# Optimization experiments

Measured on AMD Instinct MI355X. Metric: run time of the kernel, lower is better.

The kernel has to match this reference:

```python
import jax, jax.numpy as jnp
import numpy as np

B, T, NIN = 32, 2048, 2
H, E, M = 256, 256, 64  # hidden, embed, attention model_dim
L = 256                  # max_output_len


def setup_inputs() -> dict:
    key = jax.random.key(0)
    ks = jax.random.split(key, 20)
    s = 0.05
    sl = jnp.sort(jax.random.randint(ks[1], (B,), 1, T + 1))[::-1]
    sl = sl.at[0].set(T)  # assert: seq_lens[0] == max_seq_len
    return {
        "sequence": jax.random.normal(ks[0], (B, T, NIN), dtype=jnp.float32),
        "seq_lens": sl.astype(jnp.int32),
        "max_output_len": L,
        # encoder input projection (Linear n_in->embed)
        "Wp": jax.random.normal(ks[2], (NIN, E)) * s,
        "bp": jnp.zeros((E,), jnp.float32),
        # encoder LSTM (torch gate order i,f,g,o)
        "W_ih_e": jax.random.normal(ks[3], (4 * H, E)) * s,
        "W_hh_e": jax.random.normal(ks[4], (4 * H, H)) * s,
        "b_ih_e": jnp.zeros((4 * H,), jnp.float32),
        "b_hh_e": jnp.zeros((4 * H,), jnp.float32),
        # decoder LSTMCell (input is previous hidden, size H)
        "W_ih_d": jax.random.normal(ks[5], (4 * H, H)) * s,
        "W_hh_d": jax.random.normal(ks[6], (4 * H, H)) * s,
        "b_ih_d": jnp.zeros((4 * H,), jnp.float32),
        "b_hh_d": jnp.zeros((4 * H,), jnp.float32),
        # scaled dot attention projections (d_q->model_dim, d_k->model_dim)
        "Wq": jax.random.normal(ks[7], (H, M)) * s,
        "bq": jnp.zeros((M,), jnp.float32),
        "Wk": jax.random.normal(ks[8], (H, M)) * s,
        "bk": jnp.zeros((M,), jnp.float32),
    }


def _lstm_cell(h, c, x, W_ih, W_hh, b_ih, b_hh):
    g = x @ W_ih.T + h @ W_hh.T + b_ih + b_hh  # [B,4H]
    i, f, gg, o = jnp.split(g, 4, axis=-1)
    c = jax.nn.sigmoid(f) * c + jax.nn.sigmoid(i) * jnp.tanh(gg)
    h = jax.nn.sigmoid(o) * jnp.tanh(c)
    return h, c


def reference(sequence, seq_lens, max_output_len, Wp, bp,
              W_ih_e, W_hh_e, b_ih_e, b_hh_e,
              W_ih_d, W_hh_d, b_ih_d, b_hh_d,
              Wq, bq, Wk, bk):
    b, t, _ = sequence.shape
    emb = sequence @ Wp + bp  # [B,T,E]

    # encoder LSTM over time (packed semantics recovered below)
    def estep(carry, x_t):
        h, c = carry
        h, c = _lstm_cell(h, c, x_t, W_ih_e, W_hh_e, b_ih_e, b_hh_e)
        return (h, c), (h, c)

    h0 = jnp.zeros((b, H), sequence.dtype)
    _, (hs, cs) = jax.lax.scan(estep, (h0, h0), emb.transpose(1, 0, 2))  # [T,B,H]

    valid = jnp.arange(t)[None, :] < seq_lens[:, None]  # [B,T]
    enc = hs.transpose(1, 0, 2) * valid[..., None]  # pad_packed zeros beyond seq_len
    bidx = jnp.arange(b)
    hT = hs[seq_lens - 1, bidx]  # final hidden at each seq's last valid step
    cT = cs[seq_lens - 1, bidx]

    # decoder: precompute K projection and mask bias (constant across steps)
    kproj = enc @ Wk + bk  # [B,T,M]
    bias = jnp.where(valid, 0.0, -1e9).astype(sequence.dtype)  # [B,T]
    scale = 1.0 / jnp.sqrt(jnp.asarray(M, sequence.dtype))

    def dstep(carry, _):
        h, c = carry
        h2, c2 = _lstm_cell(h, c, h, W_ih_d, W_hh_d, b_ih_d, b_hh_d)
        q = h2 @ Wq + bq  # [B,M]
        scores = jnp.einsum('bm,btm->bt', q, kproj) * scale + bias
        probs = jax.nn.softmax(scores, axis=-1)  # [B,T]
        return (h2, c2), probs

    _, ptrs = jax.lax.scan(dstep, (hT, cT), None, length=max_output_len)  # [L,B,T]
    return ptrs.transpose(1, 0, 2)  # [B,L,T]
```

## Files before the change

kernel.cpp:

```cpp
#include <hip/hip_runtime.h>
#include <stdint.h>

#define B_ 32
#define T_ 2048
#define H_ 256
#define M_ 64
#define L_ 256
#define G4_ 1024

#define NG_ 8
#define NSL_ 16
#define EPT_ 16

#define SENT_ 0xFFFFFFFFu

__device__ __forceinline__ float sig_fast(float x){ return 1.f/(1.f+__expf(-x)); }
__device__ __forceinline__ float tanh_fast(float x){ return 2.f/(1.f+__expf(-2.f*x)) - 1.f; }
__device__ __forceinline__ float dot4(float4 a, float4 b){
  return fmaf(a.x,b.x, fmaf(a.y,b.y, fmaf(a.z,b.z, a.w*b.w)));
}

__global__ void prep_wdc(const float* __restrict__ a, const float* __restrict__ b,
                         float* __restrict__ o){
  int i = blockIdx.x*256 + threadIdx.x;
  o[i] = a[i] + b[i];
}

__global__ void prep_small(const float* __restrict__ Wp, const float* __restrict__ bp,
                           const float* __restrict__ Wihe, const float* __restrict__ bihe,
                           const float* __restrict__ bhhe, const float* __restrict__ bihd,
                           const float* __restrict__ bhhd, const float* __restrict__ Wq,
                           float* __restrict__ Wc0, float* __restrict__ Wc1,
                           float* __restrict__ bc, float* __restrict__ bdc,
                           float* __restrict__ WqT){
  int idx = blockIdx.x*256 + threadIdx.x;
  if (idx < 16384){
    int m = idx >> 8, k = idx & 255;
    WqT[m*256 + k] = Wq[k*64 + m];
  } else if (idx < 16384 + 1024){
    int j = idx - 16384;
    const float* wr = Wihe + j*256;
    float a0=0.f, a1=0.f, ab=0.f;
    for (int e=0;e<256;e++){
      float w = wr[e];
      a0 = fmaf(Wp[e],     w, a0);
      a1 = fmaf(Wp[256+e], w, a1);
      ab = fmaf(bp[e],     w, ab);
    }
    Wc0[j] = a0; Wc1[j] = a1;
    bc[j]  = ab + bihe[j] + bhhe[j];
    bdc[j] = bihd[j] + bhhd[j];
  }
}

__device__ __forceinline__ float2 poll8(const float* src){
  unsigned long long u;
  do {
    u = __hip_atomic_load((const unsigned long long*)src,
                          __ATOMIC_RELAXED, __HIP_MEMORY_SCOPE_AGENT);
  } while ((unsigned)u == SENT_ || (unsigned)(u>>32) == SENT_);
  return __builtin_bit_cast(float2, u);
}

__global__ __launch_bounds__(1024) void enc_kernel(
    const float* __restrict__ seq, const int* __restrict__ slen,
    const float* __restrict__ Whh,
    const float* __restrict__ Wc0, const float* __restrict__ Wc1,
    const float* __restrict__ bc,
    float* __restrict__ h_all, float* __restrict__ cT)
{
  const int tid = threadIdx.x;
  const int grp = blockIdx.x & 7, slice = blockIdx.x >> 3;
  const int rp = tid >> 4, kc = tid & 15;
  const int j = ((rp >> 4) << 8) + slice*EPT_ + (rp & 15);
  float4 w0 = *(const float4*)(Whh + (size_t)j*256 +   0 + kc*4);
  float4 w1 = *(const float4*)(Whh + (size_t)j*256 +  64 + kc*4);
  float4 w2 = *(const float4*)(Whh + (size_t)j*256 + 128 + kc*4);
  float4 w3 = *(const float4*)(Whh + (size_t)j*256 + 192 + kc*4);
  float c0 = Wc0[j], c1 = Wc1[j], cbv = bc[j];

  __shared__ float hbuf[4][256];
  __shared__ float sbuf[4][2];
  __shared__ float gbuf[4][64];

  const int ub = tid >> 4, ue = tid & 15;
  float creg = 0.f;
  int myb = 0, mylen = -1;
  if (tid < 64){ myb = grp + 8*ub; mylen = slen[myb]; }

  const int tb = tid >> 7, kp = tid & 127;
  const int stage_b = grp + 8*tb;

  for (int t = 0; t < T_; ++t){
    if (tid < 512){
      if (t == 0){
        *(float2*)&hbuf[tb][kp*2] = make_float2(0.f, 0.f);
      } else {
        *(float2*)&hbuf[tb][kp*2] =
            poll8(h_all + ((size_t)(t-1)*B_ + stage_b)*H_ + kp*2);
      }
      if (tid < 8) sbuf[tid>>1][tid&1] = seq[((size_t)(grp + 8*(tid>>1))*T_ + t)*2 + (tid&1)];
    }
    __syncthreads();

#pragma unroll
    for (int i = 0; i < 4; ++i){
      float4 h0 = *(const float4*)&hbuf[i][       kc*4];
      float4 h1 = *(const float4*)&hbuf[i][ 64 + kc*4];
      float4 h2 = *(const float4*)&hbuf[i][128 + kc*4];
      float4 h3 = *(const float4*)&hbuf[i][192 + kc*4];
      float a = dot4(w0,h0) + dot4(w1,h1) + dot4(w2,h2) + dot4(w3,h3);
#pragma unroll
      for (int off = 1; off < 16; off <<= 1) a += __shfl_xor(a, off);
      if (kc == 0)
        gbuf[i][rp] = fmaf(sbuf[i][0], c0, fmaf(sbuf[i][1], c1, a + cbv));
    }
    __syncthreads();

    if (tid < 64){
      float gi = gbuf[ub][      ue];
      float gf = gbuf[ub][16 + ue];
      float gg = gbuf[ub][32 + ue];
      float go = gbuf[ub][48 + ue];
      creg = sig_fast(gf)*creg + sig_fast(gi)*tanh_fast(gg);
      float h = sig_fast(go)*tanh_fast(creg);
      __hip_atomic_store(h_all + ((size_t)t*B_ + myb)*H_ + slice*EPT_ + ue, h,
                         __ATOMIC_RELAXED, __HIP_MEMORY_SCOPE_AGENT);
      if (t == mylen - 1) cT[myb*H_ + slice*EPT_ + ue] = creg;
    }
  }
}

__global__ __launch_bounds__(1024) void dec_kernel(
    const int* __restrict__ slen,
    const float* __restrict__ Wdc, const float* __restrict__ bdc,
    const float* __restrict__ h_all, const float* __restrict__ cT,
    float* __restrict__ h2_all)
{
  const int tid = threadIdx.x;
  const int grp = blockIdx.x & 7, slice = blockIdx.x >> 3;
  const int rp = tid >> 4, kc = tid & 15;
  const int j = ((rp >> 4) << 8) + slice*EPT_ + (rp & 15);
  float4 w0 = *(const float4*)(Wdc + (size_t)j*256 +   0 + kc*4);
  float4 w1 = *(const float4*)(Wdc + (size_t)j*256 +  64 + kc*4);
  float4 w2 = *(const float4*)(Wdc + (size_t)j*256 + 128 + kc*4);
  float4 w3 = *(const float4*)(Wdc + (size_t)j*256 + 192 + kc*4);
  float cbv = bdc[j];

  __shared__ float hbuf[4][256];
  __shared__ float gbuf[4][64];

  const int ub = tid >> 4, ue = tid & 15;
  float creg = 0.f; int myb = 0;
  if (tid < 64){ myb = grp + 8*ub; creg = cT[myb*H_ + slice*EPT_ + ue]; }

  const int tb = tid >> 7, kp = tid & 127;
  const int stage_b = grp + 8*tb;
  int stage_len = 1;
  if (tid < 512) stage_len = slen[stage_b];

  for (int s = 0; s < L_; ++s){
    if (tid < 512){
      if (s == 0){
        *(float2*)&hbuf[tb][kp*2] =
            *(const float2*)(h_all + ((size_t)(stage_len-1)*B_ + stage_b)*H_ + kp*2);
      } else {
        *(float2*)&hbuf[tb][kp*2] =
            poll8(h2_all + ((size_t)(s-1)*B_ + stage_b)*H_ + kp*2);
      }
    }
    __syncthreads();

#pragma unroll
    for (int i = 0; i < 4; ++i){
      float4 h0 = *(const float4*)&hbuf[i][       kc*4];
      float4 h1 = *(const float4*)&hbuf[i][ 64 + kc*4];
      float4 h2 = *(const float4*)&hbuf[i][128 + kc*4];
      float4 h3 = *(const float4*)&hbuf[i][192 + kc*4];
      float a = dot4(w0,h0) + dot4(w1,h1) + dot4(w2,h2) + dot4(w3,h3);
#pragma unroll
      for (int off = 1; off < 16; off <<= 1) a += __shfl_xor(a, off);
      if (kc == 0) gbuf[i][rp] = a + cbv;
    }
    __syncthreads();

    if (tid < 64){
      float gi = gbuf[ub][      ue];
      float gf = gbuf[ub][16 + ue];
      float gg = gbuf[ub][32 + ue];
      float go = gbuf[ub][48 + ue];
      creg = sig_fast(gf)*creg + sig_fast(gi)*tanh_fast(gg);
      float h = sig_fast(go)*tanh_fast(creg);
      __hip_atomic_store(h2_all + ((size_t)s*B_ + myb)*H_ + slice*EPT_ + ue, h,
                         __ATOMIC_RELAXED, __HIP_MEMORY_SCOPE_AGENT);
    }
  }
}

__global__ __launch_bounds__(256) void kproj_kernel(
    const float* __restrict__ h_all, const int* __restrict__ slen,
    const float* __restrict__ Wk, const float* __restrict__ bk,
    float* __restrict__ kp)
{
  __shared__ float wk[256*64];
  const int tid = threadIdx.x;
  const int b = blockIdx.x >> 4, tc = blockIdx.x & 15;
  const int t0 = tc*128;
#pragma unroll
  for (int i=0;i<16;i++){
    int idx = tid + i*256;
    *(float4*)(&wk[idx*4]) = *(const float4*)(Wk + idx*4);
  }
  __syncthreads();
  const int tp = tid>>2, mc = (tid&3)*16;
  const int ta = t0 + tp*2, tb = ta+1;
  const int len = slen[b];
  const bool va = ta < len, vb = tb < len;
  const float* ha = h_all + ((size_t)ta*B_ + b)*H_;
  const float* hb = h_all + ((size_t)tb*B_ + b)*H_;
  float4 A[4], Bv[4];
#pragma unroll
  for (int u=0;u<4;u++){ A[u].x=A[u].y=A[u].z=A[u].w=0.f; Bv[u]=A[u]; }

  for (int k4=0;k4<64;k4++){
    float xa[4], xb[4];
    if (va){ float4 v = *(const float4*)(ha + k4*4); xa[0]=v.x; xa[1]=v.y; xa[2]=v.z; xa[3]=v.w; }
    else   { xa[0]=xa[1]=xa[2]=xa[3]=0.f; }
    if (vb){ float4 v = *(const float4*)(hb + k4*4); xb[0]=v.x; xb[1]=v.y; xb[2]=v.z; xb[3]=v.w; }
    else   { xb[0]=xb[1]=xb[2]=xb[3]=0.f; }
#pragma unroll
    for (int jj=0;jj<4;jj++){
      const float* wr = &wk[(k4*4+jj)*64 + mc];
#pragma unroll
      for (int u=0;u<4;u++){
        float4 wv = *(const float4*)(wr + u*4);
        A[u].x  = fmaf(xa[jj],wv.x,A[u].x);  A[u].y  = fmaf(xa[jj],wv.y,A[u].y);
        A[u].z  = fmaf(xa[jj],wv.z,A[u].z);  A[u].w  = fmaf(xa[jj],wv.w,A[u].w);
        Bv[u].x = fmaf(xb[jj],wv.x,Bv[u].x); Bv[u].y = fmaf(xb[jj],wv.y,Bv[u].y);
        Bv[u].z = fmaf(xb[jj],wv.z,Bv[u].z); Bv[u].w = fmaf(xb[jj],wv.w,Bv[u].w);
      }
    }
  }
#pragma unroll
  for (int u=0;u<4;u++){
    float4 bkv = *(const float4*)(bk + mc + u*4);
    float4 ra, rb;
    ra.x = va ? A[u].x+bkv.x : bkv.x;  ra.y = va ? A[u].y+bkv.y : bkv.y;
    ra.z = va ? A[u].z+bkv.z : bkv.z;  ra.w = va ? A[u].w+bkv.w : bkv.w;
    rb.x = vb ? Bv[u].x+bkv.x : bkv.x; rb.y = vb ? Bv[u].y+bkv.y : bkv.y;
    rb.z = vb ? Bv[u].z+bkv.z : bkv.z; rb.w = vb ? Bv[u].w+bkv.w : bkv.w;
    *(float4*)(kp + ((size_t)b*T_+ta)*M_ + mc + u*4) = ra;
    *(float4*)(kp + ((size_t)b*T_+tb)*M_ + mc + u*4) = rb;
  }
}

__global__ __launch_bounds__(256) void attn_kernel(
    const float* __restrict__ h2_all, const float* __restrict__ kp,
    const float* __restrict__ WqT, const float* __restrict__ bq,
    const int* __restrict__ slen, float* __restrict__ out)
{
  const int tid = threadIdx.x;
  const int b = blockIdx.x >> 5, scg = blockIdx.x & 31;
  const int s0 = scg*8;
  __shared__ float qL[8][64];
  __shared__ float red[8][4];
  const int wid = tid>>6, lane = tid&63;

  {
    const int jj = tid>>5, mh = tid&31;
    const float* hr = h2_all + ((size_t)(s0+jj)*B_ + b)*H_;
    const float* wa = WqT + (size_t)mh*256;
    const float* wb = WqT + (size_t)(mh+32)*256;
    float a0=0.f, a1=0.f;
    for (int k4=0;k4<64;k4++){
      float4 h4 = *(const float4*)(hr + k4*4);
      float4 v0 = *(const float4*)(wa + k4*4);
      float4 v1 = *(const float4*)(wb + k4*4);
      a0 += dot4(h4,v0);
      a1 += dot4(h4,v1);
    }
    qL[jj][mh]    = a0 + bq[mh];
    qL[jj][mh+32] = a1 + bq[mh+32];
  }
  __syncthreads();

  const int len = slen[b];
  float sc_[8][8];
#pragma unroll
  for (int ti=0; ti<8; ti++){
    const int t = ti*256 + tid;
    const float* kr = kp + ((size_t)b*T_ + t)*M_;
    float tmp[8];
#pragma unroll
    for (int jj=0;jj<8;jj++) tmp[jj]=0.f;
#pragma unroll
    for (int u4=0; u4<4; u4++){
      float4 k0 = *(const float4*)(kr + u4*16);
      float4 k1 = *(const float4*)(kr + u4*16 + 4);
      float4 k2 = *(const float4*)(kr + u4*16 + 8);
      float4 k3 = *(const float4*)(kr + u4*16 + 12);
#pragma unroll
      for (int jj=0;jj<8;jj++){
        const float4* q4 = (const float4*)&qL[jj][u4*16];
        tmp[jj] += dot4(k0,q4[0]) + dot4(k1,q4[1]) + dot4(k2,q4[2]) + dot4(k3,q4[3]);
      }
    }
    float bias = (t<len) ? 0.f : -1e9f;
#pragma unroll
    for (int jj=0;jj<8;jj++) sc_[ti][jj] = fmaf(tmp[jj], 0.125f, bias);
  }

  float mx[8];
#pragma unroll
  for (int jj=0;jj<8;jj++){
    float m = sc_[0][jj];
#pragma unroll
    for (int ti=1;ti<8;ti++) m = fmaxf(m, sc_[ti][jj]);
#pragma unroll
    for (int off=1; off<64; off<<=1) m = fmaxf(m, __shfl_xor(m, off));
    if (lane==0) red[jj][wid] = m;
  }
  __syncthreads();
#pragma unroll
  for (int jj=0;jj<8;jj++)
    mx[jj] = fmaxf(fmaxf(red[jj][0],red[jj][1]), fmaxf(red[jj][2],red[jj][3]));
  __syncthreads();
#pragma unroll
  for (int jj=0;jj<8;jj++){
    float s = 0.f;
#pragma unroll
    for (int ti=0;ti<8;ti++){
      float e = __expf(sc_[ti][jj] - mx[jj]);
      sc_[ti][jj] = e;
      s += e;
    }
#pragma unroll
    for (int off=1; off<64; off<<=1) s += __shfl_xor(s, off);
    if (lane==0) red[jj][wid] = s;
  }
  __syncthreads();
#pragma unroll
  for (int jj=0;jj<8;jj++){
    float r = 1.f/(red[jj][0]+red[jj][1]+red[jj][2]+red[jj][3]);
    float* o = out + ((size_t)b*L_ + s0 + jj)*T_;
#pragma unroll
    for (int ti=0;ti<8;ti++) o[ti*256 + tid] = sc_[ti][jj]*r;
  }
}

extern "C" void kernel_launch(void* const* d_in, const int* in_sizes, int n_in,
                              void* d_out, int out_size, void* d_ws, size_t ws_size,
                              hipStream_t stream) {
  (void)in_sizes; (void)n_in; (void)out_size;
  const float* seq  = (const float*)d_in[0];
  const int*   slen = (const int*)  d_in[1];
  const float* Wp   = (const float*)d_in[3];
  const float* bp   = (const float*)d_in[4];
  const float* Wihe = (const float*)d_in[5];
  const float* Whhe = (const float*)d_in[6];
  const float* bihe = (const float*)d_in[7];
  const float* bhhe = (const float*)d_in[8];
  const float* Wihd = (const float*)d_in[9];
  const float* Whhd = (const float*)d_in[10];
  const float* bihd = (const float*)d_in[11];
  const float* bhhd = (const float*)d_in[12];
  const float* Wq   = (const float*)d_in[13];
  const float* bq   = (const float*)d_in[14];
  const float* Wk   = (const float*)d_in[15];
  const float* bk   = (const float*)d_in[16];
  float* out = (float*)d_out;

  char* p = (char*)d_ws;
  auto take = [&](size_t bytes)->char* {
    char* r = p; p += (bytes + 255) & ~(size_t)255; return r;
  };
  float* h2_all = (float*)take((size_t)L_*B_*H_*4);
  float* kproj  = (float*)take((size_t)B_*T_*M_*4);
  float* cT     = (float*)take((size_t)B_*H_*4);
  float* W_dc   = (float*)take((size_t)G4_*H_*4);
  float* Wc0    = (float*)take(G4_*4);
  float* Wc1    = (float*)take(G4_*4);
  float* bc     = (float*)take(G4_*4);
  float* b_dc   = (float*)take(G4_*4);
  float* WqT    = (float*)take((size_t)M_*H_*4);

  size_t used = (size_t)(p - (char*)d_ws);
  float* h_all;
  if (ws_size >= used + (size_t)T_*B_*H_*4) {
    h_all = (float*)take((size_t)T_*B_*H_*4);
  } else {
    h_all = out;
  }

  hipMemsetAsync(h_all,  0xFF, (size_t)T_*B_*H_*4, stream);
  hipMemsetAsync(h2_all, 0xFF, (size_t)L_*B_*H_*4, stream);

  prep_wdc  <<<G4_*H_/256, 256, 0, stream>>>(Wihd, Whhd, W_dc);
  prep_small<<<68, 256, 0, stream>>>(Wp, bp, Wihe, bihe, bhhe, bihd, bhhd, Wq,
                                     Wc0, Wc1, bc, b_dc, WqT);
  enc_kernel<<<NG_*NSL_, 1024, 0, stream>>>(seq, slen, Whhe, Wc0, Wc1, bc,
                                            h_all, cT);
  kproj_kernel<<<B_*16, 256, 0, stream>>>(h_all, slen, Wk, bk, kproj);
  dec_kernel<<<NG_*NSL_, 1024, 0, stream>>>(slen, W_dc, b_dc, h_all, cT, h2_all);
  attn_kernel<<<B_*32, 256, 0, stream>>>(h2_all, kproj, WqT, bq, slen, out);
}
```

Baseline: 7.475 ms.

## Replace sentinel polling on full history with step-tagged ring buffers

The encoder and decoder recurrences previously polled the full h_all/h2_all histories for a 0xFF sentinel, which required memsetting about 72 MB before each run. Each step's hidden state is now also published into a small per-group ring of 64-bit words tagging the value with its step index, and readers spin on that tag. Results are still written to h_all/h2_all with plain stores for the downstream kernels. This removes the large memsets and keeps the polled data in a small, L2-resident region, at the cost of 1024 threads polling 8-byte words each step instead of 512 threads.

```diff
diff --git a/kernel.cpp b/kernel.cpp
--- a/kernel.cpp
+++ b/kernel.cpp
@@ -11,8 +11,7 @@
 #define NG_ 8
 #define NSL_ 16
 #define EPT_ 16
-
-#define SENT_ 0xFFFFFFFFu
+#define RING_ 8
 
 __device__ __forceinline__ float sig_fast(float x){ return 1.f/(1.f+__expf(-x)); }
 __device__ __forceinline__ float tanh_fast(float x){ return 2.f/(1.f+__expf(-2.f*x)) - 1.f; }
@@ -53,21 +52,13 @@
   }
 }
 
-__device__ __forceinline__ float2 poll8(const float* src){
-  unsigned long long u;
-  do {
-    u = __hip_atomic_load((const unsigned long long*)src,
-                          __ATOMIC_RELAXED, __HIP_MEMORY_SCOPE_AGENT);
-  } while ((unsigned)u == SENT_ || (unsigned)(u>>32) == SENT_);
-  return __builtin_bit_cast(float2, u);
-}
-
 __global__ __launch_bounds__(1024) void enc_kernel(
     const float* __restrict__ seq, const int* __restrict__ slen,
     const float* __restrict__ Whh,
     const float* __restrict__ Wc0, const float* __restrict__ Wc1,
     const float* __restrict__ bc,
-    float* __restrict__ h_all, float* __restrict__ cT)
+    float* __restrict__ h_all, float* __restrict__ cT,
+    unsigned long long* __restrict__ ring)
 {
   const int tid = threadIdx.x;
   const int grp = blockIdx.x & 7, slice = blockIdx.x >> 3;
@@ -88,19 +79,20 @@
   int myb = 0, mylen = -1;
   if (tid < 64){ myb = grp + 8*ub; mylen = slen[myb]; }
 
-  const int tb = tid >> 7, kp = tid & 127;
-  const int stage_b = grp + 8*tb;
+  const int ib = tid >> 8, ik = tid & 255;
+  unsigned long long* ringg = ring + (size_t)grp * (RING_*1024);
 
   for (int t = 0; t < T_; ++t){
-    if (tid < 512){
-      if (t == 0){
-        *(float2*)&hbuf[tb][kp*2] = make_float2(0.f, 0.f);
-      } else {
-        *(float2*)&hbuf[tb][kp*2] =
-            poll8(h_all + ((size_t)(t-1)*B_ + stage_b)*H_ + kp*2);
-      }
-      if (tid < 8) sbuf[tid>>1][tid&1] = seq[((size_t)(grp + 8*(tid>>1))*T_ + t)*2 + (tid&1)];
-    }
+    if (t == 0){
+      hbuf[ib][ik] = 0.f;
+    } else {
+      const unsigned long long* pp = ringg + (size_t)((t-1) & (RING_-1))*1024 + tid;
+      unsigned long long v;
+      do { v = __hip_atomic_load(pp, __ATOMIC_RELAXED, __HIP_MEMORY_SCOPE_AGENT); }
+      while ((unsigned)(v >> 32) != (unsigned)t);
+      hbuf[ib][ik] = __uint_as_float((unsigned)v);
+    }
+    if (tid < 8) sbuf[tid>>1][tid&1] = seq[((size_t)(grp + 8*(tid>>1))*T_ + t)*2 + (tid&1)];
     __syncthreads();
 
 #pragma unroll
@@ -124,8 +116,11 @@
       float go = gbuf[ub][48 + ue];
       creg = sig_fast(gf)*creg + sig_fast(gi)*tanh_fast(gg);
       float h = sig_fast(go)*tanh_fast(creg);
-      __hip_atomic_store(h_all + ((size_t)t*B_ + myb)*H_ + slice*EPT_ + ue, h,
-                         __ATOMIC_RELAXED, __HIP_MEMORY_SCOPE_AGENT);
+      unsigned long long pk = ((unsigned long long)(unsigned)(t+1) << 32)
+                            | (unsigned long long)__float_as_uint(h);
+      __hip_atomic_store(ringg + (size_t)(t & (RING_-1))*1024 + ub*256 + slice*EPT_ + ue,
+                         pk, __ATOMIC_RELAXED, __HIP_MEMORY_SCOPE_AGENT);
+      h_all[((size_t)t*B_ + myb)*H_ + slice*EPT_ + ue] = h;
       if (t == mylen - 1) cT[myb*H_ + slice*EPT_ + ue] = creg;
     }
   }
@@ -135,7 +130,7 @@
     const int* __restrict__ slen,
     const float* __restrict__ Wdc, const float* __restrict__ bdc,
     const float* __restrict__ h_all, const float* __restrict__ cT,
-    float* __restrict__ h2_all)
+    float* __restrict__ h2_all, unsigned long long* __restrict__ ring)
 {
   const int tid = threadIdx.x;
   const int grp = blockIdx.x & 7, slice = blockIdx.x >> 3;
@@ -154,20 +149,20 @@
   float creg = 0.f; int myb = 0;
   if (tid < 64){ myb = grp + 8*ub; creg = cT[myb*H_ + slice*EPT_ + ue]; }
 
-  const int tb = tid >> 7, kp = tid & 127;
-  const int stage_b = grp + 8*tb;
-  int stage_len = 1;
-  if (tid < 512) stage_len = slen[stage_b];
+  const int ib = tid >> 8, ik = tid & 255;
+  const int stage_b = grp + 8*ib;
+  const int stage_len = slen[stage_b];
+  unsigned long long* ringg = ring + (size_t)grp * (RING_*1024);
 
   for (int s = 0; s < L_; ++s){
-    if (tid < 512){
-      if (s == 0){
-        *(float2*)&hbuf[tb][kp*2] =
-            *(const float2*)(h_all + ((size_t)(stage_len-1)*B_ + stage_b)*H_ + kp*2);
-      } else {
-        *(float2*)&hbuf[tb][kp*2] =
-            poll8(h2_all + ((size_t)(s-1)*B_ + stage_b)*H_ + kp*2);
-      }
+    if (s == 0){
+      hbuf[ib][ik] = h_all[((size_t)(stage_len-1)*B_ + stage_b)*H_ + ik];
+    } else {
+      const unsigned long long* pp = ringg + (size_t)((s-1) & (RING_-1))*1024 + tid;
+      unsigned long long v;
+      do { v = __hip_atomic_load(pp, __ATOMIC_RELAXED, __HIP_MEMORY_SCOPE_AGENT); }
+      while ((unsigned)(v >> 32) != (unsigned)s);
+      hbuf[ib][ik] = __uint_as_float((unsigned)v);
     }
     __syncthreads();
 
@@ -191,8 +186,11 @@
       float go = gbuf[ub][48 + ue];
       creg = sig_fast(gf)*creg + sig_fast(gi)*tanh_fast(gg);
       float h = sig_fast(go)*tanh_fast(creg);
-      __hip_atomic_store(h2_all + ((size_t)s*B_ + myb)*H_ + slice*EPT_ + ue, h,
-                         __ATOMIC_RELAXED, __HIP_MEMORY_SCOPE_AGENT);
+      unsigned long long pk = ((unsigned long long)(unsigned)(s+1) << 32)
+                            | (unsigned long long)__float_as_uint(h);
+      __hip_atomic_store(ringg + (size_t)(s & (RING_-1))*1024 + ub*256 + slice*EPT_ + ue,
+                         pk, __ATOMIC_RELAXED, __HIP_MEMORY_SCOPE_AGENT);
+      h2_all[((size_t)s*B_ + myb)*H_ + slice*EPT_ + ue] = h;
     }
   }
 }
@@ -383,6 +381,8 @@
   float* bc     = (float*)take(G4_*4);
   float* b_dc   = (float*)take(G4_*4);
   float* WqT    = (float*)take((size_t)M_*H_*4);
+  unsigned long long* ring_e = (unsigned long long*)take((size_t)NG_*RING_*1024*8);
+  unsigned long long* ring_d = (unsigned long long*)take((size_t)NG_*RING_*1024*8);
 
   size_t used = (size_t)(p - (char*)d_ws);
   float* h_all;
@@ -392,15 +392,16 @@
     h_all = out;
   }
 
-  hipMemsetAsync(h_all,  0xFF, (size_t)T_*B_*H_*4, stream);
-  hipMemsetAsync(h2_all, 0xFF, (size_t)L_*B_*H_*4, stream);
+  hipMemsetAsync(ring_e, 0, (size_t)NG_*RING_*1024*8, stream);
+  hipMemsetAsync(ring_d, 0, (size_t)NG_*RING_*1024*8, stream);
 
   prep_wdc  <<<G4_*H_/256, 256, 0, stream>>>(Wihd, Whhd, W_dc);
   prep_small<<<68, 256, 0, stream>>>(Wp, bp, Wihe, bihe, bhhe, bihd, bhhd, Wq,
                                      Wc0, Wc1, bc, b_dc, WqT);
   enc_kernel<<<NG_*NSL_, 1024, 0, stream>>>(seq, slen, Whhe, Wc0, Wc1, bc,
-                                            h_all, cT);
+                                            h_all, cT, ring_e);
   kproj_kernel<<<B_*16, 256, 0, stream>>>(h_all, slen, Wk, bk, kproj);
-  dec_kernel<<<NG_*NSL_, 1024, 0, stream>>>(slen, W_dc, b_dc, h_all, cT, h2_all);
+  dec_kernel<<<NG_*NSL_, 1024, 0, stream>>>(slen, W_dc, b_dc, h_all, cT,
+                                            h2_all, ring_d);
   attn_kernel<<<B_*32, 256, 0, stream>>>(h2_all, kproj, WqT, bq, slen, out);
 }
```

New measurement: 6.799 ms. -9.0%, faster.

## Replace sentinel polling with flag-based ring buffer exchange in recurrent LSTM kernels

Applied to the files above, without the earlier changes.

The encoder and decoder recurrences stop spinning on sentinel values in the full hidden-state history. Each block now publishes its hidden slice into a small ring buffer in global memory and raises a per-producer flag with release semantics. Consumers wait on the flags with acquire, then do one relaxed read per element, and the block's own slice is taken from shared memory. This removes the large sentinel memsets and the per-element spin loads, but adds extra barriers per step and relies on flag-ordering correctness across the ring.

```diff
diff --git a/kernel.cpp b/kernel.cpp
--- a/kernel.cpp
+++ b/kernel.cpp
@@ -11,8 +11,7 @@
 #define NG_ 8
 #define NSL_ 16
 #define EPT_ 16
-
-#define SENT_ 0xFFFFFFFFu
+#define RING_ 8
 
 __device__ __forceinline__ float sig_fast(float x){ return 1.f/(1.f+__expf(-x)); }
 __device__ __forceinline__ float tanh_fast(float x){ return 2.f/(1.f+__expf(-2.f*x)) - 1.f; }
@@ -53,21 +52,13 @@
   }
 }
 
-__device__ __forceinline__ float2 poll8(const float* src){
-  unsigned long long u;
-  do {
-    u = __hip_atomic_load((const unsigned long long*)src,
-                          __ATOMIC_RELAXED, __HIP_MEMORY_SCOPE_AGENT);
-  } while ((unsigned)u == SENT_ || (unsigned)(u>>32) == SENT_);
-  return __builtin_bit_cast(float2, u);
-}
-
 __global__ __launch_bounds__(1024) void enc_kernel(
     const float* __restrict__ seq, const int* __restrict__ slen,
     const float* __restrict__ Whh,
     const float* __restrict__ Wc0, const float* __restrict__ Wc1,
     const float* __restrict__ bc,
-    float* __restrict__ h_all, float* __restrict__ cT)
+    float* __restrict__ h_all, float* __restrict__ cT,
+    unsigned long long* __restrict__ rde, int* __restrict__ flge)
 {
   const int tid = threadIdx.x;
   const int grp = blockIdx.x & 7, slice = blockIdx.x >> 3;
@@ -82,6 +73,7 @@
   __shared__ float hbuf[4][256];
   __shared__ float sbuf[4][2];
   __shared__ float gbuf[4][64];
+  __shared__ float xbuf[4][16];
 
   const int ub = tid >> 4, ue = tid & 15;
   float creg = 0.f;
@@ -89,45 +81,80 @@
   if (tid < 64){ myb = grp + 8*ub; mylen = slen[myb]; }
 
   const int tb = tid >> 7, kp = tid & 127;
-  const int stage_b = grp + 8*tb;
-
-  for (int t = 0; t < T_; ++t){
-    if (tid < 512){
-      if (t == 0){
-        *(float2*)&hbuf[tb][kp*2] = make_float2(0.f, 0.f);
-      } else {
-        *(float2*)&hbuf[tb][kp*2] =
-            poll8(h_all + ((size_t)(t-1)*B_ + stage_b)*H_ + kp*2);
-      }
-      if (tid < 8) sbuf[tid>>1][tid&1] = seq[((size_t)(grp + 8*(tid>>1))*T_ + t)*2 + (tid&1)];
-    }
-    __syncthreads();
-
-#pragma unroll
-    for (int i = 0; i < 4; ++i){
-      float4 h0 = *(const float4*)&hbuf[i][       kc*4];
-      float4 h1 = *(const float4*)&hbuf[i][ 64 + kc*4];
-      float4 h2 = *(const float4*)&hbuf[i][128 + kc*4];
-      float4 h3 = *(const float4*)&hbuf[i][192 + kc*4];
-      float a = dot4(w0,h0) + dot4(w1,h1) + dot4(w2,h2) + dot4(w3,h3);
-#pragma unroll
-      for (int off = 1; off < 16; off <<= 1) a += __shfl_xor(a, off);
-      if (kc == 0)
-        gbuf[i][rp] = fmaf(sbuf[i][0], c0, fmaf(sbuf[i][1], c1, a + cbv));
-    }
-    __syncthreads();
-
-    if (tid < 64){
+  const int ps = (tid - 64) >> 2, pb = (tid - 64) & 3;
+
+  for (int i = 0; i < T_; ++i){
+    const int slot = (i - 1) & (RING_ - 1);
+    if (i > 0 && tid < 64){
       float gi = gbuf[ub][      ue];
       float gf = gbuf[ub][16 + ue];
       float gg = gbuf[ub][32 + ue];
       float go = gbuf[ub][48 + ue];
       creg = sig_fast(gf)*creg + sig_fast(gi)*tanh_fast(gg);
       float h = sig_fast(go)*tanh_fast(creg);
-      __hip_atomic_store(h_all + ((size_t)t*B_ + myb)*H_ + slice*EPT_ + ue, h,
-                         __ATOMIC_RELAXED, __HIP_MEMORY_SCOPE_AGENT);
-      if (t == mylen - 1) cT[myb*H_ + slice*EPT_ + ue] = creg;
-    }
+      xbuf[ub][ue] = h;
+      hbuf[ub][slice*EPT_ + ue] = h;
+      h_all[((size_t)(i-1)*B_ + myb)*H_ + slice*EPT_ + ue] = h;
+      if (i == mylen) cT[myb*H_ + slice*EPT_ + ue] = creg;
+    }
+    __syncthreads();
+
+    if (i > 0 && tid < 4){
+      unsigned long long* dst = rde + (((size_t)slot*NG_ + grp)*4 + tid)*128 + slice*8;
+      const unsigned long long* xs = (const unsigned long long*)xbuf[tid];
+#pragma unroll
+      for (int k = 0; k < 8; ++k)
+        __hip_atomic_store(dst + k, xs[k], __ATOMIC_RELAXED, __HIP_MEMORY_SCOPE_AGENT);
+      int* fp = flge + ((((size_t)slot*NG_ + grp)*NSL_ + slice)*4 + tid)*16;
+      __hip_atomic_store(fp, i, __ATOMIC_RELEASE, __HIP_MEMORY_SCOPE_AGENT);
+    }
+    if (i > 0 && tid >= 64 && tid < 128 && ps != slice){
+      const int* fp = flge + ((((size_t)slot*NG_ + grp)*NSL_ + ps)*4 + pb)*16;
+      while (__hip_atomic_load(fp, __ATOMIC_RELAXED, __HIP_MEMORY_SCOPE_AGENT) != i) {}
+      __builtin_amdgcn_fence(__ATOMIC_ACQUIRE, "agent");
+    }
+    if (tid >= 128 && tid < 136){
+      int b4 = (tid - 128) >> 1, ix = (tid - 128) & 1;
+      sbuf[b4][ix] = seq[((size_t)(grp + 8*b4)*T_ + i)*2 + ix];
+    }
+    __syncthreads();
+
+    if (tid < 512){
+      if (i == 0){
+        *(float2*)&hbuf[tb][kp*2] = make_float2(0.f, 0.f);
+      } else if ((kp >> 3) != slice){
+        unsigned long long v = __hip_atomic_load(
+            rde + (((size_t)slot*NG_ + grp)*4 + tb)*128 + kp,
+            __ATOMIC_RELAXED, __HIP_MEMORY_SCOPE_AGENT);
+        *(float2*)&hbuf[tb][kp*2] = __builtin_bit_cast(float2, v);
+      }
+    }
+    __syncthreads();
+
+#pragma unroll
+    for (int b4 = 0; b4 < 4; ++b4){
+      float4 h0 = *(const float4*)&hbuf[b4][       kc*4];
+      float4 h1 = *(const float4*)&hbuf[b4][ 64 + kc*4];
+      float4 h2 = *(const float4*)&hbuf[b4][128 + kc*4];
+      float4 h3 = *(const float4*)&hbuf[b4][192 + kc*4];
+      float a = dot4(w0,h0) + dot4(w1,h1) + dot4(w2,h2) + dot4(w3,h3);
+#pragma unroll
+      for (int off = 1; off < 16; off <<= 1) a += __shfl_xor(a, off);
+      if (kc == 0)
+        gbuf[b4][rp] = fmaf(sbuf[b4][0], c0, fmaf(sbuf[b4][1], c1, a + cbv));
+    }
+    __syncthreads();
+  }
+
+  if (tid < 64){
+    float gi = gbuf[ub][      ue];
+    float gf = gbuf[ub][16 + ue];
+    float gg = gbuf[ub][32 + ue];
+    float go = gbuf[ub][48 + ue];
+    creg = sig_fast(gf)*creg + sig_fast(gi)*tanh_fast(gg);
+    float h = sig_fast(go)*tanh_fast(creg);
+    h_all[((size_t)(T_-1)*B_ + myb)*H_ + slice*EPT_ + ue] = h;
+    if (mylen == T_) cT[myb*H_ + slice*EPT_ + ue] = creg;
   }
 }
 
@@ -135,7 +162,8 @@
     const int* __restrict__ slen,
     const float* __restrict__ Wdc, const float* __restrict__ bdc,
     const float* __restrict__ h_all, const float* __restrict__ cT,
-    float* __restrict__ h2_all)
+    float* __restrict__ h2_all,
+    unsigned long long* __restrict__ rdd, int* __restrict__ flgd)
 {
   const int tid = threadIdx.x;
   const int grp = blockIdx.x & 7, slice = blockIdx.x >> 3;
@@ -149,6 +177,7 @@
 
   __shared__ float hbuf[4][256];
   __shared__ float gbuf[4][64];
+  __shared__ float xbuf[4][16];
 
   const int ub = tid >> 4, ue = tid & 15;
   float creg = 0.f; int myb = 0;
@@ -158,42 +187,74 @@
   const int stage_b = grp + 8*tb;
   int stage_len = 1;
   if (tid < 512) stage_len = slen[stage_b];
-
-  for (int s = 0; s < L_; ++s){
-    if (tid < 512){
-      if (s == 0){
-        *(float2*)&hbuf[tb][kp*2] =
-            *(const float2*)(h_all + ((size_t)(stage_len-1)*B_ + stage_b)*H_ + kp*2);
-      } else {
-        *(float2*)&hbuf[tb][kp*2] =
-            poll8(h2_all + ((size_t)(s-1)*B_ + stage_b)*H_ + kp*2);
-      }
-    }
-    __syncthreads();
-
-#pragma unroll
-    for (int i = 0; i < 4; ++i){
-      float4 h0 = *(const float4*)&hbuf[i][       kc*4];
-      float4 h1 = *(const float4*)&hbuf[i][ 64 + kc*4];
-      float4 h2 = *(const float4*)&hbuf[i][128 + kc*4];
-      float4 h3 = *(const float4*)&hbuf[i][192 + kc*4];
-      float a = dot4(w0,h0) + dot4(w1,h1) + dot4(w2,h2) + dot4(w3,h3);
-#pragma unroll
-      for (int off = 1; off < 16; off <<= 1) a += __shfl_xor(a, off);
-      if (kc == 0) gbuf[i][rp] = a + cbv;
-    }
-    __syncthreads();
-
-    if (tid < 64){
+  const int ps = (tid - 64) >> 2, pb = (tid - 64) & 3;
+
+  for (int i = 0; i < L_; ++i){
+    const int slot = (i - 1) & (RING_ - 1);
+    if (i > 0 && tid < 64){
       float gi = gbuf[ub][      ue];
       float gf = gbuf[ub][16 + ue];
       float gg = gbuf[ub][32 + ue];
       float go = gbuf[ub][48 + ue];
       creg = sig_fast(gf)*creg + sig_fast(gi)*tanh_fast(gg);
       float h = sig_fast(go)*tanh_fast(creg);
-      __hip_atomic_store(h2_all + ((size_t)s*B_ + myb)*H_ + slice*EPT_ + ue, h,
-                         __ATOMIC_RELAXED, __HIP_MEMORY_SCOPE_AGENT);
-    }
+      xbuf[ub][ue] = h;
+      hbuf[ub][slice*EPT_ + ue] = h;
+      h2_all[((size_t)(i-1)*B_ + myb)*H_ + slice*EPT_ + ue] = h;
+    }
+    __syncthreads();
+
+    if (i > 0 && tid < 4){
+      unsigned long long* dst = rdd + (((size_t)slot*NG_ + grp)*4 + tid)*128 + slice*8;
+      const unsigned long long* xs = (const unsigned long long*)xbuf[tid];
+#pragma unroll
+      for (int k = 0; k < 8; ++k)
+        __hip_atomic_store(dst + k, xs[k], __ATOMIC_RELAXED, __HIP_MEMORY_SCOPE_AGENT);
+      int* fp = flgd + ((((size_t)slot*NG_ + grp)*NSL_ + slice)*4 + tid)*16;
+      __hip_atomic_store(fp, i, __ATOMIC_RELEASE, __HIP_MEMORY_SCOPE_AGENT);
+    }
+    if (i > 0 && tid >= 64 && tid < 128 && ps != slice){
+      const int* fp = flgd + ((((size_t)slot*NG_ + grp)*NSL_ + ps)*4 + pb)*16;
+      while (__hip_atomic_load(fp, __ATOMIC_RELAXED, __HIP_MEMORY_SCOPE_AGENT) != i) {}
+      __builtin_amdgcn_fence(__ATOMIC_ACQUIRE, "agent");
+    }
+    __syncthreads();
+
+    if (tid < 512){
+      if (i == 0){
+        *(float2*)&hbuf[tb][kp*2] =
+            *(const float2*)(h_all + ((size_t)(stage_len-1)*B_ + stage_b)*H_ + kp*2);
+      } else if ((kp >> 3) != slice){
+        unsigned long long v = __hip_atomic_load(
+            rdd + (((size_t)slot*NG_ + grp)*4 + tb)*128 + kp,
+            __ATOMIC_RELAXED, __HIP_MEMORY_SCOPE_AGENT);
+        *(float2*)&hbuf[tb][kp*2] = __builtin_bit_cast(float2, v);
+      }
+    }
+    __syncthreads();
+
+#pragma unroll
+    for (int b4 = 0; b4 < 4; ++b4){
+      float4 h0 = *(const float4*)&hbuf[b4][       kc*4];
+      float4 h1 = *(const float4*)&hbuf[b4][ 64 + kc*4];
+      float4 h2 = *(const float4*)&hbuf[b4][128 + kc*4];
+      float4 h3 = *(const float4*)&hbuf[b4][192 + kc*4];
+      float a = dot4(w0,h0) + dot4(w1,h1) + dot4(w2,h2) + dot4(w3,h3);
+#pragma unroll
+      for (int off = 1; off < 16; off <<= 1) a += __shfl_xor(a, off);
+      if (kc == 0) gbuf[b4][rp] = a + cbv;
+    }
+    __syncthreads();
+  }
+
+  if (tid < 64){
+    float gi = gbuf[ub][      ue];
+    float gf = gbuf[ub][16 + ue];
+    float gg = gbuf[ub][32 + ue];
+    float go = gbuf[ub][48 + ue];
+    creg = sig_fast(gf)*creg + sig_fast(gi)*tanh_fast(gg);
+    float h = sig_fast(go)*tanh_fast(creg);
+    h2_all[((size_t)(L_-1)*B_ + myb)*H_ + slice*EPT_ + ue] = h;
   }
 }
 
@@ -383,6 +444,10 @@
   float* bc     = (float*)take(G4_*4);
   float* b_dc   = (float*)take(G4_*4);
   float* WqT    = (float*)take((size_t)M_*H_*4);
+  unsigned long long* rde = (unsigned long long*)take((size_t)RING_*NG_*4*128*8);
+  unsigned long long* rdd = (unsigned long long*)take((size_t)RING_*NG_*4*128*8);
+  int* flge = (int*)take((size_t)RING_*NG_*NSL_*4*16*4);
+  int* flgd = (int*)take((size_t)RING_*NG_*NSL_*4*16*4);
 
   size_t used = (size_t)(p - (char*)d_ws);
   float* h_all;
@@ -392,15 +457,16 @@
     h_all = out;
   }
 
-  hipMemsetAsync(h_all,  0xFF, (size_t)T_*B_*H_*4, stream);
-  hipMemsetAsync(h2_all, 0xFF, (size_t)L_*B_*H_*4, stream);
+  hipMemsetAsync(flge, 0, (size_t)RING_*NG_*NSL_*4*16*4, stream);
+  hipMemsetAsync(flgd, 0, (size_t)RING_*NG_*NSL_*4*16*4, stream);
 
   prep_wdc  <<<G4_*H_/256, 256, 0, stream>>>(Wihd, Whhd, W_dc);
   prep_small<<<68, 256, 0, stream>>>(Wp, bp, Wihe, bihe, bhhe, bihd, bhhd, Wq,
                                      Wc0, Wc1, bc, b_dc, WqT);
   enc_kernel<<<NG_*NSL_, 1024, 0, stream>>>(seq, slen, Whhe, Wc0, Wc1, bc,
-                                            h_all, cT);
+                                            h_all, cT, rde, flge);
   kproj_kernel<<<B_*16, 256, 0, stream>>>(h_all, slen, Wk, bk, kproj);
-  dec_kernel<<<NG_*NSL_, 1024, 0, stream>>>(slen, W_dc, b_dc, h_all, cT, h2_all);
+  dec_kernel<<<NG_*NSL_, 1024, 0, stream>>>(slen, W_dc, b_dc, h_all, cT,
+                                            h2_all, rdd, flgd);
   attn_kernel<<<B_*32, 256, 0, stream>>>(h2_all, kproj, WqT, bq, slen, out);
 }
```

Measured after the change: 11.92 ms. 1.59x slower.
